# Performance work log

Measured on AMD Instinct MI355X. Metric: run time of the kernel, lower is better.

Reference implementation:

```python
import jax, jax.numpy as jnp
import numpy as np

T, B, IN, OUT, N_MOD, K = 1024, 8, 1024, 1024, 16, 2

def setup_inputs() -> dict:
    key = jax.random.key(0)
    k1, k2, k3, k4 = jax.random.split(key, 4)
    x = jax.random.normal(k1, (T, B, IN), dtype=jnp.float32)
    selection = jax.random.randint(k2, (B, K), 0, N_MOD, dtype=jnp.int64)
    weight = jax.random.normal(k3, (N_MOD, IN, OUT), dtype=jnp.float32) * (1.0 / np.sqrt(IN))
    bias = jax.random.normal(k4, (N_MOD, OUT), dtype=jnp.float32) * 0.02
    return {"x": x, "selection": selection, "weight": weight, "bias": bias}

def reference(x, selection, weight, bias):
    # time_major=True: x is [T, B, in] -> batch-major [B, T, in]
    xb = jnp.swapaxes(x, 0, 1)
    # Gather the K selected expert weight matrices per batch row: [B, K, in, out]
    W_sel = weight[selection]
    # Equivalent to matmul(x[i], cat(weight[sel], dim=1)): [B, T, K, out]
    o = jnp.einsum('bti,bkio->btko', xb, W_sel)
    Bn, Tn, Kn, On = o.shape
    o = o.reshape(Bn, Tn, Kn * On)
    # concat_dim == 1 bias: bias[sel].view(1, -1) -> [1, K*out], broadcast over T
    o = o + bias[selection].reshape(Bn, 1, Kn * On)
    # back to time-major [T, B, K*out]
    return jnp.swapaxes(o, 0, 1)
```

## Files before the change

### kernel.cpp

```cpp
#include <hip/hip_runtime.h>

#define T_DIM 1024
#define B_DIM 8
#define IN_DIM 1024
#define OUT_DIM 1024
#define N_MODL 16
#define K_SEL 2

typedef unsigned short ushort_t;
typedef __bf16 bf16x8 __attribute__((ext_vector_type(8)));
typedef float f32x4 __attribute__((ext_vector_type(4)));

__device__ __forceinline__ unsigned int f2bf2(float lo, float hi) {
  union { float f; unsigned int u; } a, b; a.f = lo; b.f = hi;
  unsigned int ra = (a.u + 0x7fffu + ((a.u >> 16) & 1u)) >> 16;
  unsigned int rb = (b.u + 0x7fffu + ((b.u >> 16) & 1u)) >> 16;
  return ra | (rb << 16);
}
__device__ __forceinline__ unsigned short f2bf(float f) {
  union { float f; unsigned int u; } v; v.f = f;
  return (unsigned short)((v.u + 0x7fffu + ((v.u >> 16) & 1u)) >> 16);
}

__device__ __forceinline__ void async_g2l(const void* g, void* l) {
  __builtin_amdgcn_global_load_lds(
      (const __attribute__((address_space(1))) unsigned int*)g,
      (__attribute__((address_space(3))) unsigned int*)l,
      16, 0, 0);
}

__global__ __launch_bounds__(256) void convert_kernel(const float* __restrict__ x,
                                                      const float* __restrict__ w,
                                                      ushort_t* __restrict__ xb,
                                                      ushort_t* __restrict__ wt) {
  __shared__ float tile[64][65];
  const int bid = blockIdx.x;
  if (bid >= 4096) {
    const int i = (bid - 4096) * 256 + threadIdx.x;
    const float4* s = (const float4*)x;
    float4 a = s[i * 2], b = s[i * 2 + 1];
    uint4 o;
    o.x = f2bf2(a.x, a.y); o.y = f2bf2(a.z, a.w);
    o.z = f2bf2(b.x, b.y); o.w = f2bf2(b.z, b.w);
    ((uint4*)xb)[i] = o;
    return;
  }
  const int m = bid >> 8;
  const int rest = bid & 255;
  const int i0 = (rest & 15) * 64;
  const int o0 = (rest >> 4) * 64;
  const float* src = w + ((size_t)m * IN_DIM + i0) * OUT_DIM + o0;
  const int c = (threadIdx.x & 15) * 4;
  const int r0 = threadIdx.x >> 4;
#pragma unroll
  for (int p = 0; p < 4; ++p) {
    const int r = r0 + p * 16;
    float4 v = *(const float4*)(src + (size_t)r * OUT_DIM + c);
    tile[r][c + 0] = v.x; tile[r][c + 1] = v.y;
    tile[r][c + 2] = v.z; tile[r][c + 3] = v.w;
  }
  __syncthreads();
  ushort_t* dst = wt + ((size_t)m * OUT_DIM + o0) * IN_DIM + i0;
#pragma unroll
  for (int p = 0; p < 4; ++p) {
    const int r = r0 + p * 16;
    ushort4 ov;
    ov.x = f2bf(tile[c + 0][r]);
    ov.y = f2bf(tile[c + 1][r]);
    ov.z = f2bf(tile[c + 2][r]);
    ov.w = f2bf(tile[c + 3][r]);
    *(ushort4*)(dst + (size_t)r * IN_DIM + c) = ov;
  }
}

__device__ __forceinline__ int read_sel(const int* __restrict__ s, int g) {
  bool i64 = true;
#pragma unroll
  for (int j = 0; j < 8; ++j) i64 &= (s[2 * j + 1] == 0);
  return i64 ? s[2 * g] : s[g];
}

__global__ __launch_bounds__(256, 2) void mlgemm_kernel(const ushort_t* __restrict__ xb,
                                                        const ushort_t* __restrict__ wt,
                                                        const int* __restrict__ selp,
                                                        const float* __restrict__ bias,
                                                        float* __restrict__ out) {
  __shared__ ushort_t As[128 * 64];
  __shared__ ushort_t Bs[2][128 * 64];

  const int b = blockIdx.z;
  const int e0 = read_sel(selp, 2 * b);
  const int e1 = read_sel(selp, 2 * b + 1);

  const ushort_t* A  = xb + (size_t)b * IN_DIM;
  const ushort_t* B0 = wt + (size_t)e0 * OUT_DIM * IN_DIM;
  const ushort_t* B1 = wt + (size_t)e1 * OUT_DIM * IN_DIM;

  const int m0 = blockIdx.y * 128;
  const int n0 = blockIdx.x * 128;

  const int lane = threadIdx.x & 63;
  const int wv = threadIdx.x >> 6;

  const int srow = lane >> 3;
  const int sx = (((lane & 7) ^ (srow & 7)) << 3);
  const ushort_t* Ab  = A  + (size_t)(m0 + srow) * (B_DIM * IN_DIM) + sx;
  const ushort_t* Bb0 = B0 + (size_t)(n0 + srow) * IN_DIM + sx;
  const ushort_t* Bb1 = B1 + (size_t)(n0 + srow) * IN_DIM + sx;

  const int frow = lane & 15;
  const int quad = lane >> 4;
  const int cbase = ((quad ^ (frow & 7)) << 3);
  const int wrow = (wv & 1) * 64;
  const int wcol = (wv >> 1) * 64;
  const ushort_t* Ard  = As    + (wrow + frow) * 64;
  const ushort_t* Brd0 = Bs[0] + (wcol + frow) * 64;
  const ushort_t* Brd1 = Bs[1] + (wcol + frow) * 64;

  f32x4 acc0[4][4] = {};
  f32x4 acc1[4][4] = {};

  for (int k0 = 0; k0 < IN_DIM; k0 += 64) {
#pragma unroll
    for (int c = 0; c < 4; ++c) {
      const int j = wv * 4 + c;
      async_g2l(Ab  + (size_t)(8 * j) * (B_DIM * IN_DIM) + k0, As + j * 512);
      async_g2l(Bb0 + (size_t)(8 * j) * IN_DIM + k0, Bs[0] + j * 512);
      async_g2l(Bb1 + (size_t)(8 * j) * IN_DIM + k0, Bs[1] + j * 512);
    }
    __syncthreads();
#pragma unroll
    for (int kk = 0; kk < 64; kk += 32) {
      const int coff = cbase ^ kk;
      bf16x8 af[4], bf0[4], bf1[4];
#pragma unroll
      for (int i = 0; i < 4; ++i) {
        af[i]  = *(const bf16x8*)(Ard  + i * 16 * 64 + coff);
        bf0[i] = *(const bf16x8*)(Brd0 + i * 16 * 64 + coff);
        bf1[i] = *(const bf16x8*)(Brd1 + i * 16 * 64 + coff);
      }
#pragma unroll
      for (int mt = 0; mt < 4; ++mt)
#pragma unroll
        for (int nt = 0; nt < 4; ++nt) {
          acc0[mt][nt] = __builtin_amdgcn_mfma_f32_16x16x32_bf16(af[mt], bf0[nt],
                                                                 acc0[mt][nt], 0, 0, 0);
          acc1[mt][nt] = __builtin_amdgcn_mfma_f32_16x16x32_bf16(af[mt], bf1[nt],
                                                                 acc1[mt][nt], 0, 0, 0);
        }
    }
    __syncthreads();
  }

  const int orow0 = m0 + wrow + quad * 4;
  const int ocol0 = n0 + wcol + frow;
  const float* bp0 = bias + (size_t)e0 * OUT_DIM;
  const float* bp1 = bias + (size_t)e1 * OUT_DIM;
  float bv0[4], bv1[4];
#pragma unroll
  for (int nt = 0; nt < 4; ++nt) {
    bv0[nt] = bp0[ocol0 + nt * 16];
    bv1[nt] = bp1[ocol0 + nt * 16];
  }
  float* C0 = out + (size_t)b * (K_SEL * OUT_DIM);
  float* C1 = C0 + OUT_DIM;
#pragma unroll
  for (int mt = 0; mt < 4; ++mt) {
#pragma unroll
    for (int r = 0; r < 4; ++r) {
      const size_t rowoff = (size_t)(orow0 + mt * 16 + r) * (B_DIM * K_SEL * OUT_DIM);
#pragma unroll
      for (int nt = 0; nt < 4; ++nt) {
        C0[rowoff + ocol0 + nt * 16] = acc0[mt][nt][r] + bv0[nt];
        C1[rowoff + ocol0 + nt * 16] = acc1[mt][nt][r] + bv1[nt];
      }
    }
  }
}

extern "C" void kernel_launch(void* const* d_in, const int* in_sizes, int n_in,
                              void* d_out, int out_size, void* d_ws, size_t ws_size,
                              hipStream_t stream) {
  const float* x    = (const float*)d_in[0];
  const int*   sel  = (const int*)d_in[1];
  const float* w    = (const float*)d_in[2];
  const float* bias = (const float*)d_in[3];
  float* out = (float*)d_out;

  ushort_t* xb = (ushort_t*)d_ws;
  ushort_t* wt = (ushort_t*)((char*)d_ws +
                             (size_t)T_DIM * B_DIM * IN_DIM * 2);

  convert_kernel<<<dim3(4096 + T_DIM * B_DIM * IN_DIM / 8 / 256), 256, 0, stream>>>(
      x, w, xb, wt);
  mlgemm_kernel<<<dim3(OUT_DIM / 128, T_DIM / 128, B_DIM), 256, 0, stream>>>(
      xb, wt, sel, bias, out);
}
```

Before: 183.5 us.

## Convert only selected experts' weights and remap GEMM grid for cache locality

The weight transpose/convert kernel now skips any expert not referenced by the selection tensor, and uses 128x128 tiles staged as bf16 in swizzled shared memory instead of a padded fp32 tile. The GEMM grid is flattened so consecutive blocks share an n-tile and differ in batch and m-tile, aiming for better L2 reuse of weight tiles. This removes conversion of unused experts (up to 16 matrices, at most 16 distinct are used from 16 selections) at the cost of redundant selection reads per block.

```diff
diff --git a/kernel.cpp b/kernel.cpp
--- a/kernel.cpp
+++ b/kernel.cpp
@@ -17,10 +17,6 @@
   unsigned int rb = (b.u + 0x7fffu + ((b.u >> 16) & 1u)) >> 16;
   return ra | (rb << 16);
 }
-__device__ __forceinline__ unsigned short f2bf(float f) {
-  union { float f; unsigned int u; } v; v.f = f;
-  return (unsigned short)((v.u + 0x7fffu + ((v.u >> 16) & 1u)) >> 16);
-}
 
 __device__ __forceinline__ void async_g2l(const void* g, void* l) {
   __builtin_amdgcn_global_load_lds(
@@ -29,14 +25,22 @@
       16, 0, 0);
 }
 
+__device__ __forceinline__ int read_sel(const int* __restrict__ s, int g) {
+  bool i64 = true;
+#pragma unroll
+  for (int j = 0; j < 8; ++j) i64 &= (s[2 * j + 1] == 0);
+  return i64 ? s[2 * g] : s[g];
+}
+
 __global__ __launch_bounds__(256) void convert_kernel(const float* __restrict__ x,
                                                       const float* __restrict__ w,
+                                                      const int* __restrict__ selp,
                                                       ushort_t* __restrict__ xb,
                                                       ushort_t* __restrict__ wt) {
-  __shared__ float tile[64][65];
+  __shared__ ushort_t tb[128 * 128];
   const int bid = blockIdx.x;
-  if (bid >= 4096) {
-    const int i = (bid - 4096) * 256 + threadIdx.x;
+  if (bid >= 1024) {
+    const int i = (bid - 1024) * 256 + threadIdx.x;
     const float4* s = (const float4*)x;
     float4 a = s[i * 2], b = s[i * 2 + 1];
     uint4 o;
@@ -45,39 +49,44 @@
     ((uint4*)xb)[i] = o;
     return;
   }
-  const int m = bid >> 8;
-  const int rest = bid & 255;
-  const int i0 = (rest & 15) * 64;
-  const int o0 = (rest >> 4) * 64;
-  const float* src = w + ((size_t)m * IN_DIM + i0) * OUT_DIM + o0;
-  const int c = (threadIdx.x & 15) * 4;
-  const int r0 = threadIdx.x >> 4;
-#pragma unroll
-  for (int p = 0; p < 4; ++p) {
-    const int r = r0 + p * 16;
-    float4 v = *(const float4*)(src + (size_t)r * OUT_DIM + c);
-    tile[r][c + 0] = v.x; tile[r][c + 1] = v.y;
-    tile[r][c + 2] = v.z; tile[r][c + 3] = v.w;
+  const int m = bid >> 6;
+  bool used = false;
+#pragma unroll
+  for (int g = 0; g < B_DIM * K_SEL; ++g) used |= (read_sel(selp, g) == m);
+  if (!used) return;
+
+  const int i0 = ((bid >> 3) & 7) * 128;
+  const int o0 = (bid & 7) * 128;
+  const float* src = w + ((size_t)(m * IN_DIM + i0)) * OUT_DIM + o0;
+
+  const int o4 = (threadIdx.x & 31) * 4;
+  const int ib = threadIdx.x >> 5;
+#pragma unroll
+  for (int p = 0; p < 16; ++p) {
+    const int i = ib + p * 8;
+    float4 v = *(const float4*)(src + (size_t)i * OUT_DIM + o4);
+    const int osw = o4 ^ (((i >> 3) & 15) << 2);
+    uint2 d2; d2.x = f2bf2(v.x, v.y); d2.y = f2bf2(v.z, v.w);
+    *(uint2*)(tb + i * 128 + osw) = d2;
   }
   __syncthreads();
-  ushort_t* dst = wt + ((size_t)m * OUT_DIM + o0) * IN_DIM + i0;
-#pragma unroll
-  for (int p = 0; p < 4; ++p) {
-    const int r = r0 + p * 16;
-    ushort4 ov;
-    ov.x = f2bf(tile[c + 0][r]);
-    ov.y = f2bf(tile[c + 1][r]);
-    ov.z = f2bf(tile[c + 2][r]);
-    ov.w = f2bf(tile[c + 3][r]);
-    *(ushort4*)(dst + (size_t)r * IN_DIM + c) = ov;
-  }
-}
-
-__device__ __forceinline__ int read_sel(const int* __restrict__ s, int g) {
-  bool i64 = true;
-#pragma unroll
-  for (int j = 0; j < 8; ++j) i64 &= (s[2 * j + 1] == 0);
-  return i64 ? s[2 * g] : s[g];
+
+  ushort_t* dst = wt + ((size_t)(m * OUT_DIM + o0)) * IN_DIM + i0;
+  const int il = (threadIdx.x & 15) * 8;
+  const int ob = threadIdx.x >> 4;
+  const int q2 = ((il >> 3) & 15) << 2;
+#pragma unroll
+  for (int p = 0; p < 8; ++p) {
+    const int o = ob + p * 16;
+    const int osw = o ^ q2;
+    uint4 d;
+    unsigned int u[8];
+#pragma unroll
+    for (int j = 0; j < 8; ++j) u[j] = tb[(il + j) * 128 + osw];
+    d.x = u[0] | (u[1] << 16); d.y = u[2] | (u[3] << 16);
+    d.z = u[4] | (u[5] << 16); d.w = u[6] | (u[7] << 16);
+    *(uint4*)(dst + (size_t)o * IN_DIM + il) = d;
+  }
 }
 
 __global__ __launch_bounds__(256, 2) void mlgemm_kernel(const ushort_t* __restrict__ xb,
@@ -88,7 +97,10 @@
   __shared__ ushort_t As[128 * 64];
   __shared__ ushort_t Bs[2][128 * 64];
 
-  const int b = blockIdx.z;
+  const int lin = blockIdx.x;
+  const int b = lin & 7;
+  const int mtile = (lin >> 3) & 7;
+  const int ntile = lin >> 6;
   const int e0 = read_sel(selp, 2 * b);
   const int e1 = read_sel(selp, 2 * b + 1);
 
@@ -96,8 +108,8 @@
   const ushort_t* B0 = wt + (size_t)e0 * OUT_DIM * IN_DIM;
   const ushort_t* B1 = wt + (size_t)e1 * OUT_DIM * IN_DIM;
 
-  const int m0 = blockIdx.y * 128;
-  const int n0 = blockIdx.x * 128;
+  const int m0 = mtile * 128;
+  const int n0 = ntile * 128;
 
   const int lane = threadIdx.x & 63;
   const int wv = threadIdx.x >> 6;
@@ -191,8 +203,7 @@
   ushort_t* wt = (ushort_t*)((char*)d_ws +
                              (size_t)T_DIM * B_DIM * IN_DIM * 2);
 
-  convert_kernel<<<dim3(4096 + T_DIM * B_DIM * IN_DIM / 8 / 256), 256, 0, stream>>>(
-      x, w, xb, wt);
-  mlgemm_kernel<<<dim3(OUT_DIM / 128, T_DIM / 128, B_DIM), 256, 0, stream>>>(
-      xb, wt, sel, bias, out);
-}
+  convert_kernel<<<dim3(1024 + T_DIM * B_DIM * IN_DIM / 8 / 256), 256, 0, stream>>>(
+      x, w, sel, xb, wt);
+  mlgemm_kernel<<<dim3(8 * 8 * B_DIM), 256, 0, stream>>>(xb, wt, sel, bias, out);
+}
```

Measured after the change: 175.9 us. -4.1%, faster.
